# Optimization experiments

Measured on AMD Instinct MI355X. Metric: run time of the kernel, lower is better.

## Reference

```python
import jax, jax.numpy as jnp
import numpy as np

K = 16
EPS = 1e-5
SLOPE = 0.01  # nn.LeakyReLU default


def _bn(x, g, b):
    # BatchNorm1d in training mode applied to [N, C, k] in torch == normalize
    # per-channel over (N, k) axes of [N, k, C] here. Biased variance (ddof=0).
    m = x.mean(axis=(0, 1))
    v = x.var(axis=(0, 1))
    return (x - m) * jax.lax.rsqrt(v + EPS) * g + b


def _lrelu(x):
    return jnp.where(x >= 0, x, SLOPE * x)


def setup_inputs() -> dict:
    key = jax.random.key(0)
    ks = jax.random.split(key, 24)
    N, CIN, COUT = 8192, 256, 256
    s = 0.05
    inp = {
        "fea_i": jax.random.normal(ks[0], (N, CIN), jnp.float32),
        "fea_last": jax.random.normal(ks[1], (N, CIN), jnp.float32),
        "xyz_i": jax.random.uniform(ks[2], (N, 3), jnp.float32),
        "xyz_last": jax.random.uniform(ks[3], (N, 3), jnp.float32),
        "t_i": jnp.float32(2.0),
        "t_last": jnp.float32(1.0),
        # lin_p: Linear(4,64) -> BN(64) -> LeakyReLU -> Linear(64,COUT)
        "wp1": jax.random.normal(ks[4], (4, 64), jnp.float32) * s,
        "bp1": jnp.zeros((64,), jnp.float32),
        "gp": jnp.ones((64,), jnp.float32),
        "bp": jnp.zeros((64,), jnp.float32),
        "wp2": jax.random.normal(ks[5], (64, COUT), jnp.float32) * s,
        "bp2": jnp.zeros((COUT,), jnp.float32),
        # lin_q / lin_k / lin_v
        "wq": jax.random.normal(ks[6], (CIN, COUT), jnp.float32) * s,
        "bq": jnp.zeros((COUT,), jnp.float32),
        "wk": jax.random.normal(ks[7], (CIN, COUT), jnp.float32) * s,
        "bk": jnp.zeros((COUT,), jnp.float32),
        "wv": jax.random.normal(ks[8], (CIN, COUT), jnp.float32) * s,
        "bv": jnp.zeros((COUT,), jnp.float32),
        # lin_w: BN -> LeakyReLU -> Linear(COUT,COUT) -> BN -> LeakyReLU
        "gw1": jnp.ones((COUT,), jnp.float32),
        "bw1": jnp.zeros((COUT,), jnp.float32),
        "ww": jax.random.normal(ks[9], (COUT, COUT), jnp.float32) * s,
        "bw": jnp.zeros((COUT,), jnp.float32),
        "gw2": jnp.ones((COUT,), jnp.float32),
        "bw2": jnp.zeros((COUT,), jnp.float32),
    }
    return inp


def reference(fea_i, fea_last, xyz_i, xyz_last, t_i, t_last,
              wp1, bp1, gp, bp, wp2, bp2,
              wq, bq, wk, bk, wv, bv,
              gw1, bw1, ww, bw, gw2, bw2):
    # k-NN: for each query point in xyz_last, K nearest points in xyz_i
    d2 = (jnp.sum(xyz_last * xyz_last, -1)[:, None]
          + jnp.sum(xyz_i * xyz_i, -1)[None, :]
          - 2.0 * xyz_last @ xyz_i.T)              # [N, N]
    idx = jax.lax.top_k(-d2, K)[1]                 # [N, K] neighbor idx into xyz_i

    fi = fea_i[idx]                                # [N, K, CIN]
    xi = xyz_i[idx]                                # [N, K, 3]
    # pe = xyzt_i - xyzt_last ; the gathered "last" side is the query point itself
    pe = jnp.concatenate([xi - xyz_last[:, None, :],
                          (t_i - t_last) * jnp.ones_like(xi[..., :1])], axis=-1)  # [N,K,4]
    pe = pe @ wp1 + bp1
    pe = _lrelu(_bn(pe, gp, bp))
    pe = pe @ wp2 + bp2                            # [N, K, COUT]

    q = fea_last @ wq + bq                         # [N, COUT], broadcast over K
    w = q[:, None, :] - (fi @ wk + bk) + pe        # [N, K, COUT]
    w = _lrelu(_bn(w, gw1, bw1))
    w = w @ ww + bw
    w = _lrelu(_bn(w, gw2, bw2))
    w = jax.nn.softmax(w, axis=1)                  # softmax over K neighbors

    v = fi @ wv + bv + pe                          # [N, K, COUT]
    return jnp.sum(w * v, axis=1)                  # [N, COUT]
```

## Files before the change

### kernel.cpp

```cpp
#include <hip/hip_runtime.h>
#include <hip/hip_bf16.h>
#include <math.h>

#define N     8192
#define KNN   16
#define NK    (N*KNN)
#define C     256
#define CH    64
#define EPS   1e-5f
#define SLOPE 0.01f

typedef __hip_bfloat16 bf16;
typedef short bfrag __attribute__((ext_vector_type(8)));
typedef float ffrag __attribute__((ext_vector_type(4)));

__device__ __forceinline__ float b2f(bf16 x){ return __bfloat162float(x); }
__device__ __forceinline__ bf16  f2b(float x){ return __float2bfloat16(x); }
__device__ __forceinline__ float b2fu(unsigned short s){
    return __uint_as_float(((unsigned)s) << 16);
}
__device__ __forceinline__ unsigned short f2bu(float x){
    union { bf16 h; unsigned short s; } u; u.h = f2b(x); return u.s;
}

union BF8 { unsigned short s[8]; uint4 u; };

template<typename T> __device__ __forceinline__ float ldv(const void* p, int i);
template<> __device__ __forceinline__ float ldv<float>(const void* p, int i){
    return ((const float*)p)[i];
}
template<> __device__ __forceinline__ float ldv<bf16>(const void* p, int i){
    return __bfloat162float(((const bf16*)p)[i]);
}
__device__ __forceinline__ bool is_f32(const void* ti){
    return ((const unsigned short*)ti)[0] == 0;
}

template<typename T>
__device__ __forceinline__ void stage8(const void* src, size_t off,
                                       unsigned short* dst){
    if (sizeof(T) == 4){
        const float4* s = (const float4*)((const float*)src + off);
        float4 a = s[0], b = s[1];
        BF8 o;
        o.s[0]=f2bu(a.x); o.s[1]=f2bu(a.y); o.s[2]=f2bu(a.z); o.s[3]=f2bu(a.w);
        o.s[4]=f2bu(b.x); o.s[5]=f2bu(b.y); o.s[6]=f2bu(b.z); o.s[7]=f2bu(b.w);
        *(uint4*)dst = o.u;
    } else {
        *(uint4*)dst = *(const uint4*)((const unsigned short*)src + off);
    }
}

__device__ __align__(256) int    g_idx[NK];
__device__ __align__(256) float  g_S[4096];
__device__ __align__(256) float  g_Rep[4*64*256];
__device__ __align__(256) float  g_M2[2048*9];
__device__ __align__(256) float4 g_pts[N];
__device__ __align__(256) unsigned short g_qT [C*C];
__device__ __align__(256) unsigned short g_kT [C*C];
__device__ __align__(256) unsigned short g_vT [C*C];
__device__ __align__(256) unsigned short g_wwT[C*C];
__device__ __align__(256) unsigned short g_p2T[C*CH];
__device__ __align__(256) unsigned short g_q  [N*C];
__device__ __align__(256) unsigned short g_fkb[N*C];
__device__ __align__(256) unsigned short g_fvb[N*C];
__device__ __align__(256) bf16   g_w1[NK*C];
__device__ __align__(256) bf16   g_vv[NK*C];
__device__ __align__(256) bf16   g_w2[NK*C];

__global__ __launch_bounds__(256) void kprepall(const void* xyz_i,
        const void* wq, const void* wk, const void* wv, const void* ww,
        const void* wp2, const void* ti_){
#pragma clang fp contract(off)
    const int b = blockIdx.x, tid = threadIdx.x;
    const bool f = is_f32(ti_);
    if (b < 64){
        int i = b*256 + tid;
        #pragma unroll
        for (int k = 0; k < 4; k++) g_Rep[i*4 + k] = 0.f;
        if (b < 16) g_S[i] = 0.f;
    } else if (b < 96){
        int p = (b-64)*256 + tid;
        float x = f ? ldv<float>(xyz_i, p*3+0) : ldv<bf16>(xyz_i, p*3+0);
        float y = f ? ldv<float>(xyz_i, p*3+1) : ldv<bf16>(xyz_i, p*3+1);
        float z = f ? ldv<float>(xyz_i, p*3+2) : ldv<bf16>(xyz_i, p*3+2);
        g_pts[p] = make_float4(x, y, z, (x*x + y*y) + z*z);
    } else {
        const void* src; unsigned short* dst; int K; int i0;
        if      (b <  352){ src=wq;  dst=g_qT;  K=256; i0=(b-  96)*256; }
        else if (b <  608){ src=wk;  dst=g_kT;  K=256; i0=(b- 352)*256; }
        else if (b <  864){ src=wv;  dst=g_vT;  K=256; i0=(b- 608)*256; }
        else if (b < 1120){ src=ww;  dst=g_wwT; K=256; i0=(b- 864)*256; }
        else              { src=wp2; dst=g_p2T; K=64;  i0=(b-1120)*256; }
        int i = i0 + tid;
        int k = i >> 8, n = i & 255;
        float v = f ? ldv<float>(src, i) : ldv<bf16>(src, i);
        dst[n*K + k] = f2bu(v);
    }
}

template<int D>
__device__ unsigned sel16(float qx, float qy, float qz, float sq, int lane){
#pragma clang fp contract(off)
    unsigned kk[D];
    #pragma unroll
    for (int i = 0; i < D; i++) kk[i] = 0xFFFFFFFFu;
    for (int t = 0; t < N/64; t++){
        float4 c = g_pts[t*64 + lane];
        float dot = (qx*c.x + qy*c.y) + qz*c.z;
        float d2  = (sq + c.w) - 2.0f*dot;
        unsigned u = __float_as_uint(d2);
        u ^= ((unsigned)(((int)u) >> 31)) | 0x80000000u;
        #pragma unroll
        for (int j = D-1; j > 0; --j){
            unsigned hi = (kk[j-1] > u) ? kk[j-1] : u;
            kk[j] = (kk[j] < hi) ? kk[j] : hi;
        }
        kk[0] = (kk[0] < u) ? kk[0] : u;
    }
    unsigned v16 = 0;
    for (int it = 0; it < 16; ++it){
        unsigned m = kk[0];
        #pragma unroll
        for (int s = 1; s < 64; s <<= 1){
            unsigned o = (unsigned)__shfl_xor((int)m, s, 64);
            m = (m < o) ? m : o;
        }
        unsigned long long ball = __ballot(kk[0] == m);
        int w = __ffsll(ball) - 1;
        if (lane == w){
            #pragma unroll
            for (int j = 0; j < D-1; j++) kk[j] = kk[j+1];
            kk[D-1] = 0xFFFFFFFFu;
        }
        v16 = m;
    }
    return v16;
}

__device__ int2 scan16(float qx, float qy, float qz, float sq, unsigned v16,
                       int lane, int* sure, int* tie){
#pragma clang fp contract(off)
    int nsure = 0, ntie = 0;
    for (int t = 0; t < N/64; t++){
        const int p = t*64 + lane;
        float4 c = g_pts[p];
        float dot = (qx*c.x + qy*c.y) + qz*c.z;
        float d2  = (sq + c.w) - 2.0f*dot;
        unsigned u = __float_as_uint(d2);
        u ^= ((unsigned)(((int)u) >> 31)) | 0x80000000u;
        bool bs = (u < v16), bt = (u == v16);
        unsigned long long Bs = __ballot(bs);
        unsigned long long Bt = __ballot(bt);
        if (bs){
            int below = __builtin_amdgcn_mbcnt_hi((unsigned)(Bs>>32),
                        __builtin_amdgcn_mbcnt_lo((unsigned)Bs, 0));
            int pos = nsure + below;
            if (pos < 16) sure[pos] = p;
        }
        if (bt){
            int below = __builtin_amdgcn_mbcnt_hi((unsigned)(Bt>>32),
                        __builtin_amdgcn_mbcnt_lo((unsigned)Bt, 0));
            int pos = ntie + below;
            if (pos < 16) tie[pos] = p;
        }
        nsure += (int)__popcll(Bs);
        ntie  += (int)__popcll(Bt);
    }
    return make_int2(nsure, ntie);
}

template<typename T>
__device__ void kknn_body(const void* xyz_last, int* sureL, int* tieL,
                          float* momL){
#pragma clang fp contract(off)
    const int lane  = threadIdx.x & 63;
    const int wslot = threadIdx.x >> 6;
    const int q     = (blockIdx.x*256 + threadIdx.x) >> 6;
    const float qx = ldv<T>(xyz_last, q*3+0);
    const float qy = ldv<T>(xyz_last, q*3+1);
    const float qz = ldv<T>(xyz_last, q*3+2);
    const float sq = (qx*qx + qy*qy) + qz*qz;
    int* sure = &sureL[wslot*16];
    int* tie  = &tieL [wslot*16];
    unsigned v16 = sel16<4>(qx, qy, qz, sq, lane);
    int2 cnt = scan16(qx, qy, qz, sq, v16, lane, sure, tie);
    if (cnt.x > 16){
        v16 = sel16<16>(qx, qy, qz, sq, lane);
        cnt = scan16(qx, qy, qz, sq, v16, lane, sure, tie);
    }
    int nsure = (cnt.x > 16) ? 16 : cnt.x;
    float dx = 0.f, dy = 0.f, dz = 0.f;
    if (lane < 16){
        int v = (lane < nsure) ? sure[lane] : tie[lane - nsure];
        if ((unsigned)v >= (unsigned)N) v = 0;
        g_idx[q*KNN + lane] = v;
        float4 c = g_pts[v];
        dx = c.x - qx; dy = c.y - qy; dz = c.z - qz;
    }
    float mm[9] = {dx, dy, dz, dx*dx, dx*dy, dx*dz, dy*dy, dy*dz, dz*dz};
    #pragma unroll
    for (int j = 0; j < 9; j++){
        #pragma unroll
        for (int s = 1; s < 16; s <<= 1)
            mm[j] += __shfl_xor(mm[j], s, 64);
    }
    if (lane == 0){
        #pragma unroll
        for (int j = 0; j < 9; j++) momL[wslot*9 + j] = mm[j];
    }
    __syncthreads();
    if (threadIdx.x < 9){
        int t = threadIdx.x;
        g_M2[blockIdx.x*9 + t] = momL[t] + momL[9+t] + momL[18+t] + momL[27+t];
    }
}
__global__ __launch_bounds__(256) void kknn(const void* xyz_last, const void* ti_){
    __shared__ int sureL[4*16];
    __shared__ int tieL [4*16];
    __shared__ float momL[4*9];
    if (is_f32(ti_)) kknn_body<float>(xyz_last, sureL, tieL, momL);
    else             kknn_body<bf16 >(xyz_last, sureL, tieL, momL);
}

template<typename T>
__device__ void kgemm3m_body(const void* A, const unsigned short* BT,
                             const void* bias, unsigned short* out,
                             unsigned short* Al, unsigned short* Bl){
    const int tid  = threadIdx.x;
    const int c0   = blockIdx.x*128, r0 = blockIdx.y*128;
    const int lane = tid & 63, wv = tid >> 6;
    const int m    = lane & 15, qd = lane >> 4;
    const int rw   = (wv >> 1)*64, cw = (wv & 1)*64;
    ffrag acc[4][4];
    #pragma unroll
    for (int i = 0; i < 4; i++)
        #pragma unroll
        for (int j = 0; j < 4; j++)
            #pragma unroll
            for (int r = 0; r < 4; r++) acc[i][j][r] = 0.f;
    const int arow = tid >> 2, ach = tid & 3;
    for (int kt = 0; kt < 8; ++kt){
        __syncthreads();
        #pragma unroll
        for (int p = 0; p < 2; ++p){
            int row = arow + p*64;
            stage8<T>(A, (size_t)(r0+row)*C + kt*32 + ach*8, &Al[row*40 + ach*8]);
            *(uint4*)&Bl[row*40 + ach*8] =
                *(const uint4*)&BT[(c0+row)*C + kt*32 + ach*8];
        }
        __syncthreads();
        bfrag af[4], bfr[4];
        #pragma unroll
        for (int i = 0; i < 4; i++)
            af[i] = *(const bfrag*)&Al[(rw + i*16 + m)*40 + qd*8];
        #pragma unroll
        for (int j = 0; j < 4; j++)
            bfr[j] = *(const bfrag*)&Bl[(cw + j*16 + m)*40 + qd*8];
        #pragma unroll
        for (int i = 0; i < 4; i++)
            #pragma unroll
            for (int j = 0; j < 4; j++)
                acc[i][j] = __builtin_amdgcn_mfma_f32_16x16x32_bf16(
                                af[i], bfr[j], acc[i][j], 0, 0, 0);
    }
    float b4[4];
    #pragma unroll
    for (int j = 0; j < 4; j++) b4[j] = ldv<T>(bias, c0 + cw + j*16 + m);
    #pragma unroll
    for (int i = 0; i < 4; i++){
        #pragma unroll
        for (int r = 0; r < 4; r++){
            int row = r0 + rw + i*16 + qd*4 + r;
            unsigned short* orow = &out[(size_t)row*C];
            #pragma unroll
            for (int j = 0; j < 4; j++)
                orow[c0 + cw + j*16 + m] = f2bu(acc[i][j][r] + b4[j]);
        }
    }
}
__global__ __launch_bounds__(256) void kgemm3m(const void* fea_i, const void* fea_last,
        const void* bq, const void* bk, const void* bv, const void* ti_){
    __shared__ unsigned short Al[128*40];
    __shared__ unsigned short Bl[128*40];
    const int which = blockIdx.z;
    const void* A = (which==0) ? fea_last : fea_i;
    const unsigned short* BT = (which==0) ? g_qT : (which==1) ? g_kT : g_vT;
    const void* bias = (which==0) ? bq : (which==1) ? bk : bv;
    unsigned short* out = (which==0) ? g_q : (which==1) ? g_fkb : g_fvb;
    if (is_f32(ti_)) kgemm3m_body<float>(A, BT, bias, out, Al, Bl);
    else             kgemm3m_body<bf16 >(A, BT, bias, out, Al, Bl);
}

template<typename T>
__device__ void kfinpe_body(const void* wp1, const void* bp1,
                            const void* gp, const void* bp_,
                            const void* t_i, const void* t_last,
                            float* mTot, float* wred){
    const int tid = threadIdx.x, lane = tid & 63, wv = tid >> 6;
    float p[9];
    #pragma unroll
    for (int j = 0; j < 9; j++) p[j] = 0.f;
    for (int i = tid; i < 2048; i += 256){
        const float* m = &g_M2[i*9];
        #pragma unroll
        for (int j = 0; j < 9; j++) p[j] += m[j];
    }
    #pragma unroll
    for (int j = 0; j < 9; j++){
        #pragma unroll
        for (int s = 1; s < 64; s <<= 1) p[j] += __shfl_xor(p[j], s, 64);
    }
    if (lane == 0){
        #pragma unroll
        for (int j = 0; j < 9; j++) wred[wv*9 + j] = p[j];
    }
    __syncthreads();
    if (tid < 9) mTot[tid] = wred[tid] + wred[9+tid] + wred[18+tid] + wred[27+tid];
    __syncthreads();
    if (tid >= 64) return;
    const int c = tid;
    float M[9];
    #pragma unroll
    for (int j = 0; j < 9; j++) M[j] = mTot[j];
    const float w0 = ldv<T>(wp1, c),     w1 = ldv<T>(wp1, 64+c);
    const float w2 = ldv<T>(wp1, 128+c), w3 = ldv<T>(wp1, 192+c);
    const float dt = ldv<T>(t_i, 0) - ldv<T>(t_last, 0);
    const float be = dt*w3 + ldv<T>(bp1, c);
    const float NKf = (float)NK;
    float lin  = w0*M[0] + w1*M[1] + w2*M[2];
    float quad = w0*w0*M[3] + w1*w1*M[6] + w2*w2*M[8]
               + 2.f*(w0*w1*M[4] + w0*w2*M[5] + w1*w2*M[7]);
    float mean = (lin + NKf*be) / NKf;
    float ev2  = (quad + 2.f*be*lin + NKf*be*be) / NKf;
    float var  = ev2 - mean*mean;
    float sc   = ldv<T>(gp, c) * rsqrtf(var + EPS);
    g_S[128+c] = sc;
    g_S[192+c] = ldv<T>(bp_, c) - mean*sc;
}
__global__ void kfinpe(const void* wp1, const void* bp1, const void* gp,
                       const void* bp_, const void* t_i, const void* t_last){
    __shared__ float mTot[9];
    __shared__ float wred[4*9];
    if (is_f32(t_i)) kfinpe_body<float>(wp1, bp1, gp, bp_, t_i, t_last, mTot, wred);
    else             kfinpe_body<bf16 >(wp1, bp1, gp, bp_, t_i, t_last, mTot, wred);
}

__global__ void kfinalize(int Cn, int outOff, const void* g, const void* b,
                          const void* ti_, int repA){
    int c = threadIdx.x;
    if (c >= Cn) return;
    float s = 0.f, ss = 0.f;
    for (int r = 0; r < 64; r++){
        s  += g_Rep[((repA  )*64 + r)*256 + c];
        ss += g_Rep[((repA+1)*64 + r)*256 + c];
    }
    bool f = is_f32(ti_);
    float mean = s / (float)NK;
    float var  = ss / (float)NK - mean*mean;
    float gv = f ? ldv<float>(g, c) : ldv<bf16>(g, c);
    float bv = f ? ldv<float>(b, c) : ldv<bf16>(b, c);
    float sc = gv * rsqrtf(var + EPS);
    g_S[outOff+c]    = sc;
    g_S[outOff+Cn+c] = bv - mean*sc;
}

template<typename T>
__device__ void kpe2m_body(const void* xyz_i, const void* xyz_last,
                           const void* wp1, const void* bp1, const void* bp2,
                           const void* t_i, const void* t_last,
                           unsigned short* Apel, unsigned short* Bpl, int* gl,
                           float* s1w, float* s2w){
    const int tid  = threadIdx.x;
    const int lane = tid & 63, wv = tid >> 6;
    const int m    = lane & 15, qd = lane >> 4;
    const int rw   = (wv >> 1)*64, cw = (wv & 1)*64;
    const int c0   = blockIdx.x*128, r0 = blockIdx.y*128;
    if (tid < 128) gl[tid] = g_idx[r0 + tid];
    { int row = tid >> 1, half = tid & 1;
      #pragma unroll
      for (int e = 0; e < 4; e++)
          *(uint4*)&Bpl[row*72 + half*32 + e*8] =
              *(const uint4*)&g_p2T[(c0+row)*CH + half*32 + e*8];
    }
    __syncthreads();
    { const int kp = lane;
      const float w0 = ldv<T>(wp1, kp),     w1 = ldv<T>(wp1, 64+kp);
      const float w2 = ldv<T>(wp1, 128+kp), w3 = ldv<T>(wp1, 192+kp);
      const float b0 = ldv<T>(bp1, kp);
      const float sc = g_S[128+kp], sh = g_S[128+64+kp];
      const float dt = ldv<T>(t_i, 0) - ldv<T>(t_last, 0);
      #pragma unroll 4
      for (int p = 0; p < 32; p++){
          int row = wv*32 + p;
          int R = r0 + row; int n = R >> 4; int g = gl[row];
          float dx = ldv<T>(xyz_i, g*3+0) - ldv<T>(xyz_last, n*3+0);
          float dy = ldv<T>(xyz_i, g*3+1) - ldv<T>(xyz_last, n*3+1);
          float dz = ldv<T>(xyz_i, g*3+2) - ldv<T>(xyz_last, n*3+2);
          float v = dx*w0 + dy*w1 + dz*w2 + dt*w3 + b0;
          v = v*sc + sh;
          v = (v >= 0.f) ? v : SLOPE*v;
          Apel[row*72 + kp] = f2bu(v);
      } }
    __syncthreads();
    ffrag acc[4][4];
    #pragma unroll
    for (int i = 0; i < 4; i++)
        #pragma unroll
        for (int j = 0; j < 4; j++)
            #pragma unroll
            for (int r = 0; r < 4; r++) acc[i][j][r] = 0.f;
    #pragma unroll
    for (int ks = 0; ks < 2; ++ks){
        bfrag af[4], bfr[4];
        #pragma unroll
        for (int i = 0; i < 4; i++)
            af[i] = *(const bfrag*)&Apel[(rw + i*16 + m)*72 + ks*32 + qd*8];
        #pragma unroll
        for (int j = 0; j < 4; j++)
            bfr[j] = *(const bfrag*)&Bpl[(cw + j*16 + m)*72 + ks*32 + qd*8];
        #pragma unroll
        for (int i = 0; i < 4; i++)
            #pragma unroll
            for (int j = 0; j < 4; j++)
                acc[i][j] = __builtin_amdgcn_mfma_f32_16x16x32_bf16(
                                af[i], bfr[j], acc[i][j], 0, 0, 0);
    }
    float bp2v[4];
    #pragma unroll
    for (int j = 0; j < 4; j++) bp2v[j] = ldv<T>(bp2, c0 + cw + j*16 + m);
    float cs[4] = {0.f,0.f,0.f,0.f}, cq[4] = {0.f,0.f,0.f,0.f};
    #pragma unroll
    for (int i = 0; i < 4; i++){
        #pragma unroll
        for (int r = 0; r < 4; r++){
            int row = rw + i*16 + qd*4 + r;
            int R = r0 + row; int n = R >> 4; int g = gl[row];
            const unsigned short* qr  = &g_q  [(size_t)n*C];
            const unsigned short* fkr = &g_fkb[(size_t)g*C];
            const unsigned short* fvr = &g_fvb[(size_t)g*C];
            #pragma unroll
            for (int j = 0; j < 4; j++){
                int col = c0 + cw + j*16 + m;
                float pe = acc[i][j][r] + bp2v[j];
                unsigned short bb = f2bu(b2fu(qr[col]) - b2fu(fkr[col]) + pe);
                ((unsigned short*)g_w1)[(size_t)R*C + col] = bb;
                float rv = b2fu(bb);
                cs[j] += rv; cq[j] += rv*rv;
                ((unsigned short*)g_vv)[(size_t)R*C + col] =
                    f2bu(b2fu(fvr[col]) + pe);
            }
        }
    }
    #pragma unroll
    for (int j = 0; j < 4; j++){
        cs[j] += __shfl_xor(cs[j], 16, 64); cs[j] += __shfl_xor(cs[j], 32, 64);
        cq[j] += __shfl_xor(cq[j], 16, 64); cq[j] += __shfl_xor(cq[j], 32, 64);
    }
    if (lane < 16){
        #pragma unroll
        for (int j = 0; j < 4; j++){
            s1w[(wv>>1)*128 + cw + j*16 + lane] = cs[j];
            s2w[(wv>>1)*128 + cw + j*16 + lane] = cq[j];
        }
    }
    __syncthreads();
    if (tid < 128){
        float a = s1w[tid] + s1w[128+tid];
        float b = s2w[tid] + s2w[128+tid];
        int rep = blockIdx.y & 63;
        atomicAdd(&g_Rep[(0*64 + rep)*256 + c0 + tid], a);
        atomicAdd(&g_Rep[(1*64 + rep)*256 + c0 + tid], b);
    }
}
__global__ __launch_bounds__(256) void kpe2m(const void* xyz_i, const void* xyz_last,
        const void* wp1, const void* bp1, const void* bp2,
        const void* t_i, const void* t_last){
    __shared__ unsigned short Apel[128*72];
    __shared__ unsigned short Bpl[128*72];
    __shared__ int gl[128];
    __shared__ float s1w[256], s2w[256];
    if (is_f32(t_i))
        kpe2m_body<float>(xyz_i, xyz_last, wp1, bp1, bp2, t_i, t_last,
                          Apel, Bpl, gl, s1w, s2w);
    else
        kpe2m_body<bf16 >(xyz_i, xyz_last, wp1, bp1, bp2, t_i, t_last,
                          Apel, Bpl, gl, s1w, s2w);
}

template<typename T>
__device__ void kgemmww_body(const void* bw, unsigned short* Al,
                             unsigned short* Bl, float* scl, float* shl,
                             float* t1w, float* t2w){
    const int tid  = threadIdx.x;
    const int c0   = blockIdx.x*128, r0 = blockIdx.y*128;
    const int lane = tid & 63, wv = tid >> 6;
    const int m    = lane & 15, qd = lane >> 4;
    const int rw   = (wv >> 1)*64, cw = (wv & 1)*64;
    scl[tid] = g_S[768 + tid]; shl[tid] = g_S[768 + C + tid];
    ffrag acc[4][4];
    #pragma unroll
    for (int i = 0; i < 4; i++)
        #pragma unroll
        for (int j = 0; j < 4; j++)
            #pragma unroll
            for (int r = 0; r < 4; r++) acc[i][j][r] = 0.f;
    const int arow = tid >> 2, ach = tid & 3;
    for (int kt = 0; kt < 8; ++kt){
        __syncthreads();
        #pragma unroll
        for (int p = 0; p < 2; ++p){
            int row = arow + p*64;
            int kk  = kt*32 + ach*8;
            BF8 in, o;
            in.u = *(const uint4*)&g_w1[(size_t)(r0+row)*C + kk];
            #pragma unroll
            for (int e = 0; e < 8; e++){
                float x = b2fu(in.s[e]);
                x = x*scl[kk+e] + shl[kk+e];
                x = (x >= 0.f) ? x : SLOPE*x;
                o.s[e] = f2bu(x);
            }
            *(uint4*)&Al[row*40 + ach*8] = o.u;
            *(uint4*)&Bl[row*40 + ach*8] =
                *(const uint4*)&g_wwT[(c0+row)*C + kt*32 + ach*8];
        }
        __syncthreads();
        bfrag af[4], bf_[4];
        #pragma unroll
        for (int i = 0; i < 4; i++)
            af[i] = *(const bfrag*)&Al[(rw + i*16 + m)*40 + qd*8];
        #pragma unroll
        for (int j = 0; j < 4; j++)
            bf_[j] = *(const bfrag*)&Bl[(cw + j*16 + m)*40 + qd*8];
        #pragma unroll
        for (int i = 0; i < 4; i++)
            #pragma unroll
            for (int j = 0; j < 4; j++)
                acc[i][j] = __builtin_amdgcn_mfma_f32_16x16x32_bf16(
                                af[i], bf_[j], acc[i][j], 0, 0, 0);
    }
    float bwv[4];
    #pragma unroll
    for (int j = 0; j < 4; j++) bwv[j] = ldv<T>(bw, c0 + cw + j*16 + m);
    float cs[4] = {0.f,0.f,0.f,0.f}, cq[4] = {0.f,0.f,0.f,0.f};
    #pragma unroll
    for (int j = 0; j < 4; j++){
        int col = c0 + cw + j*16 + m;
        #pragma unroll
        for (int i = 0; i < 4; i++){
            #pragma unroll
            for (int r = 0; r < 4; r++){
                int row = r0 + rw + i*16 + qd*4 + r;
                unsigned short bb = f2bu(acc[i][j][r] + bwv[j]);
                ((unsigned short*)g_w2)[(size_t)row*C + col] = bb;
                float rv = b2fu(bb);
                cs[j] += rv; cq[j] += rv*rv;
            }
        }
    }
    #pragma unroll
    for (int j = 0; j < 4; j++){
        cs[j] += __shfl_xor(cs[j], 16, 64); cs[j] += __shfl_xor(cs[j], 32, 64);
        cq[j] += __shfl_xor(cq[j], 16, 64); cq[j] += __shfl_xor(cq[j], 32, 64);
    }
    if (lane < 16){
        #pragma unroll
        for (int j = 0; j < 4; j++){
            t1w[(wv>>1)*128 + cw + j*16 + lane] = cs[j];
            t2w[(wv>>1)*128 + cw + j*16 + lane] = cq[j];
        }
    }
    __syncthreads();
    if (tid < 128){
        float a = t1w[tid] + t1w[128+tid];
        float b = t2w[tid] + t2w[128+tid];
        int rep = blockIdx.y & 63;
        atomicAdd(&g_Rep[(2*64 + rep)*256 + c0 + tid], a);
        atomicAdd(&g_Rep[(3*64 + rep)*256 + c0 + tid], b);
    }
}
__global__ __launch_bounds__(256) void kgemmww(const void* bw, const void* ti_){
    __shared__ unsigned short Al[128*40];
    __shared__ unsigned short Bl[128*40];
    __shared__ float scl[C], shl[C];
    __shared__ float t1w[256], t2w[256];
    if (is_f32(ti_)) kgemmww_body<float>(bw, Al, Bl, scl, shl, t1w, t2w);
    else             kgemmww_body<bf16 >(bw, Al, Bl, scl, shl, t1w, t2w);
}

__global__ __launch_bounds__(256) void kfinal(void* out, const void* ti_){
    const int n = blockIdx.x, c = threadIdx.x;
    const float sc = g_S[1792+c], sh = g_S[1792+C+c];
    float u[KNN];
    float m = -3.4e38f;
    #pragma unroll
    for (int k = 0; k < KNN; k++){
        float x = b2f(g_w2[(size_t)(n*KNN+k)*C + c])*sc + sh;
        x = (x >= 0.f) ? x : SLOPE*x;
        u[k] = x; m = fmaxf(m, x);
    }
    float ssum = 0.f, o = 0.f;
    #pragma unroll
    for (int k = 0; k < KNN; k++){
        float e = __expf(u[k] - m);
        ssum += e;
        o += e * b2f(g_vv[(size_t)(n*KNN+k)*C + c]);
    }
    float r = o / ssum;
    if (is_f32(ti_)) ((float*)out)[(size_t)n*C + c] = r;
    else             ((bf16*)out)[(size_t)n*C + c] = f2b(r);
}

extern "C" void kernel_launch(void* const* d_in, const int* in_sizes, int n_in,
                              void* d_out, int out_size, void* d_ws, size_t ws_size,
                              hipStream_t stream){
    const void* fea_i    = d_in[0];
    const void* fea_last = d_in[1];
    const void* xyz_i    = d_in[2];
    const void* xyz_last = d_in[3];
    const void* t_i      = d_in[4];
    const void* t_last   = d_in[5];
    const void* wp1 = d_in[6];
    const void* bp1 = d_in[7];
    const void* gp  = d_in[8];
    const void* bp_ = d_in[9];
    const void* wp2 = d_in[10];
    const void* bp2 = d_in[11];
    const void* wq  = d_in[12];
    const void* bq  = d_in[13];
    const void* wk  = d_in[14];
    const void* bk  = d_in[15];
    const void* wv  = d_in[16];
    const void* bv  = d_in[17];
    const void* gw1 = d_in[18];
    const void* bw1 = d_in[19];
    const void* ww  = d_in[20];
    const void* bw  = d_in[21];
    const void* gw2 = d_in[22];
    const void* bw2 = d_in[23];

    kprepall<<<1184, 256, 0, stream>>>(xyz_i, wq, wk, wv, ww, wp2, t_i);
    kknn<<<N/4, 256, 0, stream>>>(xyz_last, t_i);
    kgemm3m<<<dim3(2, 64, 3), 256, 0, stream>>>(fea_i, fea_last, bq, bk, bv, t_i);
    kfinpe<<<1, 256, 0, stream>>>(wp1, bp1, gp, bp_, t_i, t_last);
    kpe2m<<<dim3(2, NK/128), 256, 0, stream>>>(xyz_i, xyz_last, wp1, bp1, bp2,
                                               t_i, t_last);
    kfinalize<<<1, 256, 0, stream>>>(256, 768, gw1, bw1, t_i, 0);
    kgemmww<<<dim3(2, NK/128), 256, 0, stream>>>(bw, t_i);
    kfinalize<<<1, 256, 0, stream>>>(256, 1792, gw2, bw2, t_i, 2);
    kfinal<<<N, 256, 0, stream>>>(d_out, t_i);
}
```

Measured before the change: 349.3 us.

## Use uniform grid spatial hashing to restrict kNN candidate search

Builds a 16^3 cell grid over xyz_i points (histogram, prefix scan, scatter into sorted order). Each query now scans only the 5x5x5 neighbouring cells (up to 512 candidates) instead of all 8192 points. It checks that the 16th distance lies inside the covered region and falls back to the full brute-force scan otherwise. Ties are sorted by index so the result matches the original ordering. This adds three small kernels and per-block shared memory for the candidate lists.

```diff
diff --git a/kernel.cpp b/kernel.cpp
--- a/kernel.cpp
+++ b/kernel.cpp
@@ -9,6 +9,7 @@
 #define CH    64
 #define EPS   1e-5f
 #define SLOPE 0.01f
+#define LISTMAX 512
 
 typedef __hip_bfloat16 bf16;
 typedef short bfrag __attribute__((ext_vector_type(8)));
@@ -51,11 +52,25 @@
     }
 }
 
+__device__ __forceinline__ int mbcnt64(unsigned long long b){
+    return __builtin_amdgcn_mbcnt_hi((unsigned)(b>>32),
+           __builtin_amdgcn_mbcnt_lo((unsigned)b, 0));
+}
+__device__ __forceinline__ unsigned d2key(float d2){
+    unsigned u = __float_as_uint(d2);
+    return u ^ (((unsigned)(((int)u) >> 31)) | 0x80000000u);
+}
+
 __device__ __align__(256) int    g_idx[NK];
 __device__ __align__(256) float  g_S[4096];
 __device__ __align__(256) float  g_Rep[4*64*256];
 __device__ __align__(256) float  g_M2[2048*9];
 __device__ __align__(256) float4 g_pts[N];
+__device__ __align__(256) int    g_cellCnt[4096];
+__device__ __align__(256) int    g_cellStart[4100];
+__device__ __align__(256) int    g_cellCur[4096];
+__device__ __align__(256) float4 g_spts[N];
+__device__ __align__(256) int    g_sidx[N];
 __device__ __align__(256) unsigned short g_qT [C*C];
 __device__ __align__(256) unsigned short g_kT [C*C];
 __device__ __align__(256) unsigned short g_vT [C*C];
@@ -68,6 +83,13 @@
 __device__ __align__(256) bf16   g_vv[NK*C];
 __device__ __align__(256) bf16   g_w2[NK*C];
 
+__device__ __forceinline__ int cell_of(float4 c){
+    int cx = (int)(c.x*16.f); cx = cx<0?0:(cx>15?15:cx);
+    int cy = (int)(c.y*16.f); cy = cy<0?0:(cy>15?15:cy);
+    int cz = (int)(c.z*16.f); cz = cz<0?0:(cz>15?15:cz);
+    return (cz<<8) | (cy<<4) | cx;
+}
+
 __global__ __launch_bounds__(256) void kprepall(const void* xyz_i,
         const void* wq, const void* wk, const void* wv, const void* ww,
         const void* wp2, const void* ti_){
@@ -79,6 +101,7 @@
         #pragma unroll
         for (int k = 0; k < 4; k++) g_Rep[i*4 + k] = 0.f;
         if (b < 16) g_S[i] = 0.f;
+        else if (b < 32) g_cellCnt[(b-16)*256 + tid] = 0;
     } else if (b < 96){
         int p = (b-64)*256 + tid;
         float x = f ? ldv<float>(xyz_i, p*3+0) : ldv<bf16>(xyz_i, p*3+0);
@@ -99,6 +122,41 @@
     }
 }
 
+__global__ __launch_bounds__(256) void khist(){
+    int p = blockIdx.x*256 + threadIdx.x;
+    atomicAdd(&g_cellCnt[cell_of(g_pts[p])], 1);
+}
+__global__ __launch_bounds__(256) void kscan(){
+    __shared__ int sc[256];
+    const int tid = threadIdx.x;
+    int carry = 0;
+    for (int ch = 0; ch < 16; ch++){
+        int i = ch*256 + tid;
+        int v = g_cellCnt[i];
+        sc[tid] = v;
+        __syncthreads();
+        for (int s = 1; s < 256; s <<= 1){
+            int t_ = (tid >= s) ? sc[tid - s] : 0;
+            __syncthreads();
+            sc[tid] += t_;
+            __syncthreads();
+        }
+        int excl = carry + sc[tid] - v;
+        g_cellStart[i] = excl;
+        g_cellCur[i]   = excl;
+        carry += sc[255];
+        __syncthreads();
+    }
+    if (tid == 0) g_cellStart[4096] = carry;
+}
+__global__ __launch_bounds__(256) void kscatter(){
+    int p = blockIdx.x*256 + threadIdx.x;
+    float4 c = g_pts[p];
+    int pos = atomicAdd(&g_cellCur[cell_of(c)], 1);
+    g_spts[pos] = c;
+    g_sidx[pos] = p;
+}
+
 template<int D>
 __device__ unsigned sel16(float qx, float qy, float qz, float sq, int lane){
 #pragma clang fp contract(off)
@@ -109,8 +167,7 @@
         float4 c = g_pts[t*64 + lane];
         float dot = (qx*c.x + qy*c.y) + qz*c.z;
         float d2  = (sq + c.w) - 2.0f*dot;
-        unsigned u = __float_as_uint(d2);
-        u ^= ((unsigned)(((int)u) >> 31)) | 0x80000000u;
+        unsigned u = d2key(d2);
         #pragma unroll
         for (int j = D-1; j > 0; --j){
             unsigned hi = (kk[j-1] > u) ? kk[j-1] : u;
@@ -147,21 +204,16 @@
         float4 c = g_pts[p];
         float dot = (qx*c.x + qy*c.y) + qz*c.z;
         float d2  = (sq + c.w) - 2.0f*dot;
-        unsigned u = __float_as_uint(d2);
-        u ^= ((unsigned)(((int)u) >> 31)) | 0x80000000u;
+        unsigned u = d2key(d2);
         bool bs = (u < v16), bt = (u == v16);
         unsigned long long Bs = __ballot(bs);
         unsigned long long Bt = __ballot(bt);
         if (bs){
-            int below = __builtin_amdgcn_mbcnt_hi((unsigned)(Bs>>32),
-                        __builtin_amdgcn_mbcnt_lo((unsigned)Bs, 0));
-            int pos = nsure + below;
+            int pos = nsure + mbcnt64(Bs);
             if (pos < 16) sure[pos] = p;
         }
         if (bt){
-            int below = __builtin_amdgcn_mbcnt_hi((unsigned)(Bt>>32),
-                        __builtin_amdgcn_mbcnt_lo((unsigned)Bt, 0));
-            int pos = ntie + below;
+            int pos = ntie + mbcnt64(Bt);
             if (pos < 16) tie[pos] = p;
         }
         nsure += (int)__popcll(Bs);
@@ -172,7 +224,7 @@
 
 template<typename T>
 __device__ void kknn_body(const void* xyz_last, int* sureL, int* tieL,
-                          float* momL){
+                          int* listL, float* momL){
 #pragma clang fp contract(off)
     const int lane  = threadIdx.x & 63;
     const int wslot = threadIdx.x >> 6;
@@ -183,19 +235,145 @@
     const float sq = (qx*qx + qy*qy) + qz*qz;
     int* sure = &sureL[wslot*16];
     int* tie  = &tieL [wslot*16];
-    unsigned v16 = sel16<4>(qx, qy, qz, sq, lane);
-    int2 cnt = scan16(qx, qy, qz, sq, v16, lane, sure, tie);
-    if (cnt.x > 16){
+    int* list = &listL[wslot*LISTMAX];
+
+    int cqx = (int)(qx*16.f); cqx = cqx<0?0:(cqx>15?15:cqx);
+    int cqy = (int)(qy*16.f); cqy = cqy<0?0:(cqy>15?15:cqy);
+    int cqz = (int)(qz*16.f); cqz = cqz<0?0:(cqz>15?15:cqz);
+
+    int cnt0 = 0, cnt1 = 0, cs0 = 0, cs1 = 0;
+    #pragma unroll
+    for (int h = 0; h < 2; h++){
+        int idx = lane*2 + h;
+        if (idx < 125){
+            int iz = idx/25, r = idx - iz*25, iy = r/5, ix = r - iy*5;
+            int cx = cqx+ix-2, cy = cqy+iy-2, cz = cqz+iz-2;
+            if ((unsigned)cx < 16u && (unsigned)cy < 16u && (unsigned)cz < 16u){
+                int cell = (cz<<8) | (cy<<4) | cx;
+                int s = g_cellStart[cell], e = g_cellStart[cell+1];
+                if (h == 0){ cs0 = s; cnt0 = e - s; }
+                else       { cs1 = s; cnt1 = e - s; }
+            }
+        }
+    }
+    int tot = cnt0 + cnt1;
+    int incl = tot;
+    #pragma unroll
+    for (int s = 1; s < 64; s <<= 1){
+        int u = __shfl_up(incl, s, 64);
+        if (lane >= s) incl += u;
+    }
+    const int Tn = __shfl(incl, 63, 64);
+    int base = incl - tot;
+    bool full = (Tn > LISTMAX) || (Tn < 16);
+    unsigned v16 = 0;
+    int nsure = 0, ntie = 0;
+    if (!full){
+        for (int i = 0; i < cnt0; i++) list[base+i] = cs0 + i;
+        for (int i = 0; i < cnt1; i++) list[base+cnt0+i] = cs1 + i;
+        unsigned kk[4] = {~0u,~0u,~0u,~0u};
+        int chunks = (Tn + 63) >> 6;
+        for (int t = 0; t < chunks; t++){
+            int li = t*64 + lane;
+            unsigned u = 0xFFFFFFFFu;
+            if (li < Tn){
+                float4 c = g_spts[list[li]];
+                float dot = (qx*c.x + qy*c.y) + qz*c.z;
+                u = d2key((sq + c.w) - 2.0f*dot);
+            }
+            #pragma unroll
+            for (int j = 3; j > 0; --j){
+                unsigned hi = (kk[j-1] > u) ? kk[j-1] : u;
+                kk[j] = (kk[j] < hi) ? kk[j] : hi;
+            }
+            kk[0] = (kk[0] < u) ? kk[0] : u;
+        }
+        for (int it = 0; it < 16; ++it){
+            unsigned m = kk[0];
+            #pragma unroll
+            for (int s = 1; s < 64; s <<= 1){
+                unsigned o = (unsigned)__shfl_xor((int)m, s, 64);
+                m = (m < o) ? m : o;
+            }
+            unsigned long long ball = __ballot(kk[0] == m);
+            int w = __ffsll(ball) - 1;
+            if (lane == w){
+                kk[0]=kk[1]; kk[1]=kk[2]; kk[2]=kk[3]; kk[3]=0xFFFFFFFFu;
+            }
+            v16 = m;
+        }
+        const float h_ = 0.0625f;
+        float dmin = 1e30f;
+        if (cqx-2 > 0)  dmin = fminf(dmin, qx - (float)(cqx-2)*h_);
+        if (cqx+3 < 16) dmin = fminf(dmin, (float)(cqx+3)*h_ - qx);
+        if (cqy-2 > 0)  dmin = fminf(dmin, qy - (float)(cqy-2)*h_);
+        if (cqy+3 < 16) dmin = fminf(dmin, (float)(cqy+3)*h_ - qy);
+        if (cqz-2 > 0)  dmin = fminf(dmin, qz - (float)(cqz-2)*h_);
+        if (cqz+3 < 16) dmin = fminf(dmin, (float)(cqz+3)*h_ - qz);
+        unsigned ub = d2key(dmin*dmin);
+        if (!(v16 < ub)) full = true;
+    }
+    if (!full){
+        int chunks = (Tn + 63) >> 6;
+        for (int t = 0; t < chunks; t++){
+            int li = t*64 + lane;
+            unsigned u = 0xFFFFFFFFu; int oi = 0;
+            if (li < Tn){
+                int pos = list[li];
+                float4 c = g_spts[pos];
+                oi = g_sidx[pos];
+                float dot = (qx*c.x + qy*c.y) + qz*c.z;
+                u = d2key((sq + c.w) - 2.0f*dot);
+            }
+            bool bs = (li < Tn) && (u < v16);
+            bool bt = (li < Tn) && (u == v16);
+            unsigned long long Bs = __ballot(bs);
+            unsigned long long Bt = __ballot(bt);
+            if (bs){
+                int pos2 = nsure + mbcnt64(Bs);
+                if (pos2 < 16) sure[pos2] = oi;
+            }
+            if (bt){
+                int pos2 = ntie + mbcnt64(Bt);
+                if (pos2 < 16) tie[pos2] = oi;
+            }
+            nsure += (int)__popcll(Bs);
+            ntie  += (int)__popcll(Bt);
+        }
+        if (nsure > 16 || (ntie > 16 && nsure < 16)) full = true;
+    }
+    const bool gridok = !full;
+    if (full){
         v16 = sel16<16>(qx, qy, qz, sq, lane);
-        cnt = scan16(qx, qy, qz, sq, v16, lane, sure, tie);
-    }
-    int nsure = (cnt.x > 16) ? 16 : cnt.x;
+        int2 c2 = scan16(qx, qy, qz, sq, v16, lane, sure, tie);
+        nsure = c2.x; ntie = c2.y;
+    }
+    if (nsure > 16) nsure = 16;
+    int vsel = 0;
+    if (lane < 16 && lane < nsure) vsel = sure[lane];
+    if (gridok){
+        int tv = (lane < (ntie < 16 ? ntie : 16)) ? tie[lane] : 0x7FFFFFFF;
+        #pragma unroll
+        for (int k = 2; k <= 16; k <<= 1)
+            #pragma unroll
+            for (int j = k>>1; j > 0; j >>= 1){
+                int o = __shfl_xor(tv, j, 64);
+                bool asc = ((lane & k) == 0);
+                bool low = ((lane & j) == 0);
+                int mn = tv < o ? tv : o;
+                int mx = tv < o ? o : tv;
+                tv = (asc == low) ? mn : mx;
+            }
+        int tfrom = __shfl(tv, (lane - nsure) & 63, 64);
+        if (lane < 16 && lane >= nsure) vsel = tfrom;
+    } else {
+        if (lane < 16 && lane >= nsure) vsel = tie[lane - nsure];
+    }
     float dx = 0.f, dy = 0.f, dz = 0.f;
     if (lane < 16){
-        int v = (lane < nsure) ? sure[lane] : tie[lane - nsure];
-        if ((unsigned)v >= (unsigned)N) v = 0;
-        g_idx[q*KNN + lane] = v;
-        float4 c = g_pts[v];
+        if ((unsigned)vsel >= (unsigned)N) vsel = 0;
+        g_idx[q*KNN + lane] = vsel;
+        float4 c = g_pts[vsel];
         dx = c.x - qx; dy = c.y - qy; dz = c.z - qz;
     }
     float mm[9] = {dx, dy, dz, dx*dx, dx*dy, dx*dz, dy*dy, dy*dz, dz*dz};
@@ -218,9 +396,10 @@
 __global__ __launch_bounds__(256) void kknn(const void* xyz_last, const void* ti_){
     __shared__ int sureL[4*16];
     __shared__ int tieL [4*16];
+    __shared__ int listL[4*LISTMAX];
     __shared__ float momL[4*9];
-    if (is_f32(ti_)) kknn_body<float>(xyz_last, sureL, tieL, momL);
-    else             kknn_body<bf16 >(xyz_last, sureL, tieL, momL);
+    if (is_f32(ti_)) kknn_body<float>(xyz_last, sureL, tieL, listL, momL);
+    else             kknn_body<bf16 >(xyz_last, sureL, tieL, listL, momL);
 }
 
 template<typename T>
@@ -641,6 +820,9 @@
     const void* bw2 = d_in[23];
 
     kprepall<<<1184, 256, 0, stream>>>(xyz_i, wq, wk, wv, ww, wp2, t_i);
+    khist<<<32, 256, 0, stream>>>();
+    kscan<<<1, 256, 0, stream>>>();
+    kscatter<<<32, 256, 0, stream>>>();
     kknn<<<N/4, 256, 0, stream>>>(xyz_last, t_i);
     kgemm3m<<<dim3(2, 64, 3), 256, 0, stream>>>(fea_i, fea_last, bq, bk, bv, t_i);
     kfinpe<<<1, 256, 0, stream>>>(wp1, bp1, gp, bp_, t_i, t_last);
```

Result: faster. 321.2 us (-8.0%).
